# Kernel tuning notes

Hardware: AMD Instinct MI355X
Metric: run time of the kernel (lower is better)

The kernel has to match this reference:

```python
import jax, jax.numpy as jnp
import numpy as np

B, T, D = 16, 2048, 256
QK = 64


def setup_inputs() -> dict:
    key = jax.random.key(0)
    ks = jax.random.split(key, 9)
    x = jax.random.normal(ks[0], (B, T, D), dtype=jnp.float32)
    sl = jax.random.uniform(ks[1], (B, T), dtype=jnp.float32)
    mask = jax.random.randint(ks[2], (B, T), 0, 2, dtype=jnp.int32)
    s = 1.0 / np.sqrt(D).astype(np.float32)
    Wq = jax.random.normal(ks[3], (QK, D), dtype=jnp.float32) * s
    bq = jnp.zeros((QK,), dtype=jnp.float32)
    Wk = jax.random.normal(ks[4], (QK, D), dtype=jnp.float32) * s
    bk = jnp.zeros((QK,), dtype=jnp.float32)
    Wv = jax.random.normal(ks[5], (D, D), dtype=jnp.float32) * s
    bv = jnp.zeros((D,), dtype=jnp.float32)
    return {"x": x, "sl": sl, "mask": mask, "Wq": Wq, "bq": bq,
            "Wk": Wk, "bk": bk, "Wv": Wv, "bv": bv}


def reference(x, sl, mask, Wq, bq, Wk, bk, Wv, bv):
    # x: [B,T,D], sl: [B,T] soft labels, mask: [B,T] valid positions
    sl = jnp.clip(sl, 0.0, 1.0)
    q = jnp.einsum('btd,ed->bte', x, Wq) + bq          # [B,T,QK]
    k = jnp.einsum('btd,ed->bte', x, Wk) + bk          # [B,T,QK]
    v = jnp.einsum('btd,ed->bte', x, Wv) + bv          # [B,T,D]
    scale = jnp.float32(1.0 / np.sqrt(QK))
    score = jnp.einsum('bte,bse->bts', q, k) * scale   # [B,T,T]
    # emotion scaling by (1 + sl_j^2) per key position j
    score = score * (1.0 + sl[:, None, :] ** 2)
    score = jnp.where(mask[:, None, :] == 0, jnp.float32(-1e9), score)
    prob = jax.nn.softmax(score, axis=-1)              # [B,T,T]
    out = jnp.einsum('bts,bsd->btd', prob, v)          # [B,T,D]
    return out.mean(axis=1)                            # [B,D]
```

## Files before the change

kernel.cpp:

```cpp
#include <hip/hip_runtime.h>
#include <stdint.h>

#define B_ 16
#define T_ 2048
#define D_ 256
#define QK_ 64
#define LOG2E 1.44269504088896340736f
#define NCH 8

typedef _Float16 f16;
typedef _Float16 f16x2 __attribute__((ext_vector_type(2)));
typedef __fp16 fp16x2 __attribute__((ext_vector_type(2)));
typedef _Float16 f16x8 __attribute__((ext_vector_type(8)));
typedef float f32x16 __attribute__((ext_vector_type(16)));

__device__ __forceinline__ float fexp2(float x) {
#if __has_builtin(__builtin_amdgcn_exp2f)
    return __builtin_amdgcn_exp2f(x);
#else
    return exp2f(x);
#endif
}
__device__ __forceinline__ float flog2(float x) {
#if __has_builtin(__builtin_amdgcn_logf)
    return __builtin_amdgcn_logf(x);
#else
    return log2f(x);
#endif
}
__device__ __forceinline__ f16x2 cvt2(float a, float b) {
#if __has_builtin(__builtin_amdgcn_cvt_pkrtz)
    fp16x2 r = __builtin_amdgcn_cvt_pkrtz(a, b);
    return __builtin_bit_cast(f16x2, r);
#else
    f16x2 r; r[0] = (f16)a; r[1] = (f16)b; return r;
#endif
}
__device__ __forceinline__ f16x8 cvt8(const float* p) {
    union { f16x2 h2[4]; f16x8 h8; } u;
    const float4 a0 = *(const float4*)p;
    const float4 a1 = *(const float4*)(p + 4);
    u.h2[0] = cvt2(a0.x, a0.y); u.h2[1] = cvt2(a0.z, a0.w);
    u.h2[2] = cvt2(a1.x, a1.y); u.h2[3] = cvt2(a1.z, a1.w);
    return u.h8;
}


__global__ __launch_bounds__(256, 4) void kP(
    const float* __restrict__ x, const float* __restrict__ sl,
    const float* __restrict__ Wq, const float* __restrict__ bq,
    const float* __restrict__ Wk, const float* __restrict__ bk,
    f16* __restrict__ qf, f16* __restrict__ kf)
{
    __shared__ __align__(16) f16 xs[32 * D_];
    __shared__ float ksc[32];
    const int tid = threadIdx.x;
    const int wv = tid >> 6, l = tid & 63, lo = l & 31, hi = l >> 5;
    const int b = blockIdx.y, tile = blockIdx.x, t0 = tile * 32;

    #pragma unroll
    for (int i = 0; i < 4; ++i) {
        const int f = i * 256 + tid;
        const int r = f >> 5, j = f & 31;
        const f16x8 h = cvt8(x + (size_t)(b * T_ + t0 + r) * D_ + j * 8);
        *(f16x8*)(xs + r * D_ + ((j ^ r) << 3)) = h;
    }
    if (tid < 32) {
        float s = sl[(size_t)b * T_ + t0 + tid];
        s = fminf(fmaxf(s, 0.f), 1.f);
        ksc[tid] = 0.125f * (1.f + s * s) * LOG2E;
    }
    __syncthreads();

    const int e = wv * 32 + lo;
    const float* wrow = ((e < 64) ? (Wq + (size_t)e * D_)
                                  : (Wk + (size_t)(e - 64) * D_)) + hi * 8;
    f32x16 acc;
    #pragma unroll
    for (int i = 0; i < 16; ++i) acc[i] = 0.f;
    #pragma unroll
    for (int ks = 0; ks < 16; ++ks) {
        const f16x8 a  = *(const f16x8*)(xs + lo * D_ + ((((ks << 1) + hi) ^ lo) << 3));
        const f16x8 bf = cvt8(wrow + ks * 16);
        acc = __builtin_amdgcn_mfma_f32_32x32x16_f16(a, bf, acc, 0, 0, 0);
    }
    const float bias = (e < 64) ? bq[e] : bk[e - 64];
    __syncthreads();
    f16* hout = xs;
    #pragma unroll
    for (int i = 0; i < 16; ++i) {
        const int row = (i & 3) + 8 * (i >> 2) + 4 * hi;
        float v = acc[i] + bias;
        if (e >= 64) v *= ksc[row];
        hout[row * 128 + e] = (f16)v;
    }
    __syncthreads();
    const int kc2 = tid >> 6, hi2 = (tid >> 5) & 1, lo2 = tid & 31;
    const f16* srcq = hout + lo2 * 128 + kc2 * 16 + hi2 * 8;
    const size_t tb = ((size_t)b * 64 + tile) * 2048 + tid * 8;
    *(f16x8*)(qf + tb) = *(const f16x8*)srcq;
    *(f16x8*)(kf + tb) = *(const f16x8*)(srcq + 64);
}

__global__ __launch_bounds__(256, 4) void kZ(
    const f16* __restrict__ qf, const f16* __restrict__ kf,
    const int* __restrict__ mask, float* __restrict__ zpart)
{
    __shared__ __align__(16) float red[128 * 32];
    const int tid = threadIdx.x;
    const int wv = tid >> 6, l = tid & 63, lo = l & 31, hi = l >> 5;
    const int b = blockIdx.y;
    const int tIdx = blockIdx.x >> 3, ckg = blockIdx.x & 7;

    const f16* abase = qf + ((size_t)b * 64 + tIdx * 4 + wv) * 2048 + l * 8;
    f16x8 a[4];
    #pragma unroll
    for (int kc = 0; kc < 4; ++kc) a[kc] = *(const f16x8*)(abase + kc * 512);

    float zp[16];
    #pragma unroll
    for (int i = 0; i < 16; ++i) zp[i] = 0.f;

    #pragma unroll
    for (int g = 0; g < 8; ++g) {
        const int stile = ckg * 8 + g;
        const float mb = mask[b * T_ + stile * 32 + lo] ? 0.f : -1e9f;
        const f16* bbase = kf + ((size_t)b * 64 + stile) * 2048 + l * 8;
        f32x16 c;
        #pragma unroll
        for (int i = 0; i < 16; ++i) c[i] = mb;
        #pragma unroll
        for (int kc = 0; kc < 4; ++kc) {
            const f16x8 bf = *(const f16x8*)(bbase + kc * 512);
            c = __builtin_amdgcn_mfma_f32_32x32x16_f16(a[kc], bf, c, 0, 0, 0);
        }
        #pragma unroll
        for (int i = 0; i < 16; ++i) zp[i] += fexp2(c[i]);
    }
    #pragma unroll
    for (int i = 0; i < 16; ++i) {
        const int row = wv * 32 + (i & 3) + 8 * (i >> 2) + 4 * hi;
        const int col = (lo & 3) | ((((lo >> 2) ^ row) & 7) << 2);
        red[row * 32 + col] = zp[i];
    }
    __syncthreads();
    if (tid < 128) {
        float s = 0.f;
        #pragma unroll
        for (int c = 0; c < 8; ++c) {
            const float4 v = *(const float4*)(red + tid * 32 + (((c ^ tid) & 7) << 2));
            s += v.x + v.y + v.z + v.w;
        }
        zpart[(size_t)(b * NCH + ckg) * T_ + tIdx * 128 + tid] = s;
    }
}

__global__ __launch_bounds__(256, 4) void kW(
    const f16* __restrict__ qf, const f16* __restrict__ kf,
    const float* __restrict__ zpart, float* __restrict__ wpart)
{
    __shared__ __align__(16) float red[128 * 32];
    __shared__ float lz_s[256];
    const int tid = threadIdx.x;
    const int wv = tid >> 6, l = tid & 63, lo = l & 31, hi = l >> 5;
    const int b = blockIdx.y;
    const int sIdx = blockIdx.x >> 3, tcg = blockIdx.x & 7;

    {
        const float* zb = zpart + (size_t)(b * NCH) * T_ + tcg * 256 + tid;
        float z = 0.f;
        #pragma unroll
        for (int ck = 0; ck < NCH; ++ck) z += zb[(size_t)ck * T_];
        lz_s[tid] = -flog2(z);
    }
    const f16* abase = kf + ((size_t)b * 64 + sIdx * 4 + wv) * 2048 + l * 8;
    f16x8 a[4];
    #pragma unroll
    for (int kc = 0; kc < 4; ++kc) a[kc] = *(const f16x8*)(abase + kc * 512);

    float wp[16];
    #pragma unroll
    for (int i = 0; i < 16; ++i) wp[i] = 0.f;
    __syncthreads();

    #pragma unroll
    for (int g = 0; g < 8; ++g) {
        const int qtile = tcg * 8 + g;
        const float bias = lz_s[g * 32 + lo];
        const f16* bbase = qf + ((size_t)b * 64 + qtile) * 2048 + l * 8;
        f32x16 c;
        #pragma unroll
        for (int i = 0; i < 16; ++i) c[i] = bias;
        #pragma unroll
        for (int kc = 0; kc < 4; ++kc) {
            const f16x8 bf = *(const f16x8*)(bbase + kc * 512);
            c = __builtin_amdgcn_mfma_f32_32x32x16_f16(a[kc], bf, c, 0, 0, 0);
        }
        #pragma unroll
        for (int i = 0; i < 16; ++i) wp[i] += fexp2(c[i]);
    }
    #pragma unroll
    for (int i = 0; i < 16; ++i) {
        const int row = wv * 32 + (i & 3) + 8 * (i >> 2) + 4 * hi;
        const int col = (lo & 3) | ((((lo >> 2) ^ row) & 7) << 2);
        red[row * 32 + col] = wp[i];
    }
    __syncthreads();
    if (tid < 128) {
        float s = 0.f;
        #pragma unroll
        for (int c = 0; c < 8; ++c) {
            const float4 v = *(const float4*)(red + tid * 32 + (((c ^ tid) & 7) << 2));
            s += v.x + v.y + v.z + v.w;
        }
        wpart[(size_t)(b * NCH + tcg) * T_ + sIdx * 128 + tid] = s;
    }
}

__global__ __launch_bounds__(256, 4) void kY(
    const float* __restrict__ x, const float* __restrict__ wpart,
    const int* __restrict__ mask, float* __restrict__ ypart,
    float* __restrict__ swp)
{
    __shared__ float wloc[32];
    const int b  = blockIdx.y;
    const int ch = blockIdx.x;
    const int tid = threadIdx.x;

    if (tid < 32) {
        const int s = ch * 32 + tid;
        const float* wb = wpart + (size_t)(b * NCH) * T_ + s;
        float v = 0.f;
        #pragma unroll
        for (int ck = 0; ck < NCH; ++ck) v += wb[(size_t)ck * T_];
        v *= mask[b * T_ + s] ? (1.f / (float)T_) : 0.f;
        wloc[tid] = v;
        float sv = v;
        #pragma unroll
        for (int off = 1; off <= 16; off <<= 1) sv += __shfl_xor(sv, off);
        if (tid == 0) swp[b * 64 + ch] = sv;
    }
    __syncthreads();
    const float* xb = x + ((size_t)b * T_ + ch * 32) * D_;
    float acc = 0.f;
    #pragma unroll 8
    for (int s = 0; s < 32; ++s) acc += wloc[s] * xb[(size_t)s * D_ + tid];
    ypart[((size_t)b * 64 + ch) * D_ + tid] = acc;
}

__global__ __launch_bounds__(256, 4) void kOUT(
    const float* __restrict__ ypart, const float* __restrict__ swp,
    const float* __restrict__ Wv, const float* __restrict__ bv,
    float* __restrict__ out)
{
    __shared__ __align__(16) float ys[D_];
    __shared__ float sw0;
    const int b   = blockIdx.x;
    const int tid = threadIdx.x;

    float yv = 0.f;
    #pragma unroll
    for (int ch = 0; ch < 64; ++ch) yv += ypart[((size_t)b * 64 + ch) * D_ + tid];
    ys[tid] = yv;
    float s = (tid < 64) ? swp[b * 64 + tid] : 0.f;
    #pragma unroll
    for (int off = 1; off <= 32; off <<= 1) s += __shfl_xor(s, off);
    if (tid == 0) sw0 = s;
    __syncthreads();
    const float sw = sw0;
    const float4* wv4 = (const float4*)(Wv + (size_t)tid * D_);
    const float4* ys4 = (const float4*)ys;
    float o = 0.f;
    #pragma unroll
    for (int i = 0; i < D_ / 4; ++i) {
        const float4 a = wv4[i];
        const float4 y = ys4[i];
        o += a.x * y.x + a.y * y.y + a.z * y.z + a.w * y.w;
    }
    out[(size_t)b * D_ + tid] = o + bv[tid] * sw;
}

extern "C" void kernel_launch(void* const* d_in, const int* in_sizes, int n_in,
                              void* d_out, int out_size, void* d_ws, size_t ws_size,
                              hipStream_t stream)
{
    const float* x    = (const float*)d_in[0];
    const float* sl   = (const float*)d_in[1];
    const int*   mask = (const int*)d_in[2];
    const float* Wq   = (const float*)d_in[3];
    const float* bq   = (const float*)d_in[4];
    const float* Wk   = (const float*)d_in[5];
    const float* bk   = (const float*)d_in[6];
    const float* Wv   = (const float*)d_in[7];
    const float* bv   = (const float*)d_in[8];
    float* out = (float*)d_out;

    f16*   qf    = (f16*)d_ws;
    f16*   kf    = qf + (size_t)B_ * T_ * QK_;
    float* zpart = (float*)(kf + (size_t)B_ * T_ * QK_);
    float* wpart = zpart + (size_t)B_ * NCH * T_;
    float* swp   = wpart + (size_t)B_ * NCH * T_;
    float* yp    = swp + B_ * 64;

    kP  <<<dim3(64, B_), 256, 0, stream>>>(x, sl, Wq, bq, Wk, bk, qf, kf);
    kZ  <<<dim3(128, B_), 256, 0, stream>>>(qf, kf, mask, zpart);
    kW  <<<dim3(128, B_), 256, 0, stream>>>(qf, kf, zpart, wpart);
    kY  <<<dim3(64, B_), 256, 0, stream>>>(x, wpart, mask, yp, swp);
    kOUT<<<dim3(B_), 256, 0, stream>>>(yp, swp, Wv, bv, out);
}
```

Baseline: 93.47 us.

## Compact unmasked keys and skip masked columns in the score kernels

Builds a per-batch prefix-sum compaction of valid key positions and gathers K rows into a dense buffer with a new kernel. The Z and W passes then loop only over tiles that hold valid keys, and blocks past the valid count exit early. This cuts the MFMA and exp work on masked columns, about half with the random mask. In exchange it adds an extra launch, a gather pass, scatter index arrays and an indirect lookup in kY. It also changes behaviour for a fully masked row.

```diff
diff --git a/kernel.cpp b/kernel.cpp
--- a/kernel.cpp
+++ b/kernel.cpp
@@ -48,12 +48,15 @@
 
 __global__ __launch_bounds__(256, 4) void kP(
     const float* __restrict__ x, const float* __restrict__ sl,
+    const int* __restrict__ mask,
     const float* __restrict__ Wq, const float* __restrict__ bq,
     const float* __restrict__ Wk, const float* __restrict__ bk,
-    f16* __restrict__ qf, f16* __restrict__ kf)
+    f16* __restrict__ qf, f16* __restrict__ kf,
+    int* __restrict__ sidx, int* __restrict__ inv, int* __restrict__ nv)
 {
     __shared__ __align__(16) f16 xs[32 * D_];
     __shared__ float ksc[32];
+    __shared__ int wtot[4];
     const int tid = threadIdx.x;
     const int wv = tid >> 6, l = tid & 63, lo = l & 31, hi = l >> 5;
     const int b = blockIdx.y, tile = blockIdx.x, t0 = tile * 32;
@@ -100,17 +103,63 @@
     const size_t tb = ((size_t)b * 64 + tile) * 2048 + tid * 8;
     *(f16x8*)(qf + tb) = *(const f16x8*)srcq;
     *(f16x8*)(kf + tb) = *(const f16x8*)(srcq + 64);
+
+    if (tile == 0) {
+        int bits = 0, c = 0;
+        #pragma unroll
+        for (int i = 0; i < 8; ++i) {
+            const int m = mask[b * T_ + tid * 8 + i] ? 1 : 0;
+            bits |= m << i; c += m;
+        }
+        int cs = c;
+        #pragma unroll
+        for (int off = 1; off < 64; off <<= 1) {
+            const int v = __shfl_up(cs, off);
+            if (l >= off) cs += v;
+        }
+        if (l == 63) wtot[wv] = cs;
+        __syncthreads();
+        int pos = cs - c;
+        #pragma unroll
+        for (int w = 0; w < 4; ++w) if (w < wv) pos += wtot[w];
+        #pragma unroll
+        for (int i = 0; i < 8; ++i)
+            if ((bits >> i) & 1) {
+                sidx[b * T_ + pos] = tid * 8 + i;
+                inv[b * T_ + tid * 8 + i] = pos;
+                ++pos;
+            }
+        if (tid == 255) nv[b] = pos;
+    }
+}
+
+__global__ __launch_bounds__(256, 4) void kG(
+    const f16* __restrict__ kf, const int* __restrict__ sidx,
+    const int* __restrict__ nv, f16* __restrict__ kfc)
+{
+    const int b = blockIdx.y, tile = blockIdx.x;
+    const int Nv = nv[b];
+    if (tile * 32 >= Nv) return;
+    const int tid = threadIdx.x;
+    const int kc = tid >> 6, hi = (tid >> 5) & 1, lo = tid & 31;
+    const int pos = tile * 32 + lo;
+    const int r = (pos < Nv) ? sidx[b * T_ + pos] : 0;
+    const f16* src = kf + ((size_t)b * 64 + (r >> 5)) * 2048
+                        + kc * 512 + hi * 256 + (r & 31) * 8;
+    *(f16x8*)(kfc + ((size_t)b * 64 + tile) * 2048 + tid * 8) = *(const f16x8*)src;
 }
 
 __global__ __launch_bounds__(256, 4) void kZ(
-    const f16* __restrict__ qf, const f16* __restrict__ kf,
-    const int* __restrict__ mask, float* __restrict__ zpart)
+    const f16* __restrict__ qf, const f16* __restrict__ kfc,
+    const int* __restrict__ nv, float* __restrict__ zpart)
 {
     __shared__ __align__(16) float red[128 * 32];
     const int tid = threadIdx.x;
     const int wv = tid >> 6, l = tid & 63, lo = l & 31, hi = l >> 5;
     const int b = blockIdx.y;
     const int tIdx = blockIdx.x >> 3, ckg = blockIdx.x & 7;
+    const int Nv = nv[b];
+    const int ntiles = (Nv + 31) >> 5;
 
     const f16* abase = qf + ((size_t)b * 64 + tIdx * 4 + wv) * 2048 + l * 8;
     f16x8 a[4];
@@ -121,11 +170,9 @@
     #pragma unroll
     for (int i = 0; i < 16; ++i) zp[i] = 0.f;
 
-    #pragma unroll
-    for (int g = 0; g < 8; ++g) {
-        const int stile = ckg * 8 + g;
-        const float mb = mask[b * T_ + stile * 32 + lo] ? 0.f : -1e9f;
-        const f16* bbase = kf + ((size_t)b * 64 + stile) * 2048 + l * 8;
+    for (int g = ckg; g < ntiles; g += 8) {
+        const float mb = (g * 32 + lo < Nv) ? 0.f : -1e9f;
+        const f16* bbase = kfc + ((size_t)b * 64 + g) * 2048 + l * 8;
         f32x16 c;
         #pragma unroll
         for (int i = 0; i < 16; ++i) c[i] = mb;
@@ -156,15 +203,18 @@
 }
 
 __global__ __launch_bounds__(256, 4) void kW(
-    const f16* __restrict__ qf, const f16* __restrict__ kf,
-    const float* __restrict__ zpart, float* __restrict__ wpart)
+    const f16* __restrict__ qf, const f16* __restrict__ kfc,
+    const int* __restrict__ nv, const float* __restrict__ zpart,
+    float* __restrict__ wpart)
 {
     __shared__ __align__(16) float red[128 * 32];
     __shared__ float lz_s[256];
-    const int tid = threadIdx.x;
-    const int wv = tid >> 6, l = tid & 63, lo = l & 31, hi = l >> 5;
     const int b = blockIdx.y;
     const int sIdx = blockIdx.x >> 3, tcg = blockIdx.x & 7;
+    const int Nv = nv[b];
+    if (sIdx * 128 >= Nv) return;
+    const int tid = threadIdx.x;
+    const int wv = tid >> 6, l = tid & 63, lo = l & 31, hi = l >> 5;
 
     {
         const float* zb = zpart + (size_t)(b * NCH) * T_ + tcg * 256 + tid;
@@ -173,7 +223,7 @@
         for (int ck = 0; ck < NCH; ++ck) z += zb[(size_t)ck * T_];
         lz_s[tid] = -flog2(z);
     }
-    const f16* abase = kf + ((size_t)b * 64 + sIdx * 4 + wv) * 2048 + l * 8;
+    const f16* abase = kfc + ((size_t)b * 64 + sIdx * 4 + wv) * 2048 + l * 8;
     f16x8 a[4];
     #pragma unroll
     for (int kc = 0; kc < 4; ++kc) a[kc] = *(const f16x8*)(abase + kc * 512);
@@ -206,7 +256,7 @@
         red[row * 32 + col] = wp[i];
     }
     __syncthreads();
-    if (tid < 128) {
+    if (tid < 128 && sIdx * 128 + tid < Nv) {
         float s = 0.f;
         #pragma unroll
         for (int c = 0; c < 8; ++c) {
@@ -219,8 +269,8 @@
 
 __global__ __launch_bounds__(256, 4) void kY(
     const float* __restrict__ x, const float* __restrict__ wpart,
-    const int* __restrict__ mask, float* __restrict__ ypart,
-    float* __restrict__ swp)
+    const int* __restrict__ mask, const int* __restrict__ inv,
+    float* __restrict__ ypart, float* __restrict__ swp)
 {
     __shared__ float wloc[32];
     const int b  = blockIdx.y;
@@ -229,11 +279,14 @@
 
     if (tid < 32) {
         const int s = ch * 32 + tid;
-        const float* wb = wpart + (size_t)(b * NCH) * T_ + s;
         float v = 0.f;
-        #pragma unroll
-        for (int ck = 0; ck < NCH; ++ck) v += wb[(size_t)ck * T_];
-        v *= mask[b * T_ + s] ? (1.f / (float)T_) : 0.f;
+        if (mask[b * T_ + s]) {
+            const int j = inv[b * T_ + s];
+            const float* wb = wpart + (size_t)(b * NCH) * T_ + j;
+            #pragma unroll
+            for (int ck = 0; ck < NCH; ++ck) v += wb[(size_t)ck * T_];
+            v *= (1.f / (float)T_);
+        }
         wloc[tid] = v;
         float sv = v;
         #pragma unroll
@@ -243,8 +296,10 @@
     __syncthreads();
     const float* xb = x + ((size_t)b * T_ + ch * 32) * D_;
     float acc = 0.f;
-    #pragma unroll 8
-    for (int s = 0; s < 32; ++s) acc += wloc[s] * xb[(size_t)s * D_ + tid];
+    for (int s = 0; s < 32; ++s) {
+        const float w = wloc[s];
+        if (w != 0.f) acc += w * xb[(size_t)s * D_ + tid];
+    }
     ypart[((size_t)b * 64 + ch) * D_ + tid] = acc;
 }
 
@@ -296,15 +351,20 @@
     float* out = (float*)d_out;
 
     f16*   qf    = (f16*)d_ws;
-    f16*   kf    = qf + (size_t)B_ * T_ * QK_;
-    float* zpart = (float*)(kf + (size_t)B_ * T_ * QK_);
+    f16*   kf    = qf  + (size_t)B_ * T_ * QK_;
+    f16*   kfc   = kf  + (size_t)B_ * T_ * QK_;
+    float* zpart = (float*)(kfc + (size_t)B_ * T_ * QK_);
     float* wpart = zpart + (size_t)B_ * NCH * T_;
-    float* swp   = wpart + (size_t)B_ * NCH * T_;
-    float* yp    = swp + B_ * 64;
-
-    kP  <<<dim3(64, B_), 256, 0, stream>>>(x, sl, Wq, bq, Wk, bk, qf, kf);
-    kZ  <<<dim3(128, B_), 256, 0, stream>>>(qf, kf, mask, zpart);
-    kW  <<<dim3(128, B_), 256, 0, stream>>>(qf, kf, zpart, wpart);
-    kY  <<<dim3(64, B_), 256, 0, stream>>>(x, wpart, mask, yp, swp);
+    float* yp    = wpart + (size_t)B_ * NCH * T_;
+    int*   sidx  = (int*)(yp + (size_t)B_ * 64 * D_);
+    int*   inv   = sidx + (size_t)B_ * T_;
+    int*   nv    = inv + (size_t)B_ * T_;
+    float* swp   = (float*)(nv + 64);
+
+    kP  <<<dim3(64, B_), 256, 0, stream>>>(x, sl, mask, Wq, bq, Wk, bk, qf, kf, sidx, inv, nv);
+    kG  <<<dim3(64, B_), 256, 0, stream>>>(kf, sidx, nv, kfc);
+    kZ  <<<dim3(128, B_), 256, 0, stream>>>(qf, kfc, nv, zpart);
+    kW  <<<dim3(128, B_), 256, 0, stream>>>(qf, kfc, nv, zpart, wpart);
+    kY  <<<dim3(64, B_), 256, 0, stream>>>(x, wpart, mask, inv, yp, swp);
     kOUT<<<dim3(B_), 256, 0, stream>>>(yp, swp, Wv, bv, out);
 }
```

New measurement: 82.74 us. 1.13x faster.
